# Optimization experiments

Hardware: AMD Instinct MI355X
Metric: run time of the kernel (lower is better)

## Reference

```python
import jax, jax.numpy as jnp
import numpy as np

T, N, F_IN, H, E, OUT = 24, 20000, 64, 256, 320000, 1


def setup_inputs() -> dict:
    key = jax.random.key(0)
    ks = jax.random.split(key, 16)
    inp = {
        "x": jax.random.normal(ks[0], (T, N, F_IN), dtype=jnp.float32),
        "edge_index": jax.random.randint(ks[1], (2, E), 0, N, dtype=jnp.int32),
        "edge_weight": jax.random.uniform(ks[2], (E,), dtype=jnp.float32),
        # GCNConv 1 (input_size -> hidden)
        "W1": jax.random.normal(ks[3], (F_IN, H), dtype=jnp.float32) / np.sqrt(F_IN),
        "b1": jnp.zeros((H,), dtype=jnp.float32),
        # GCNConv 2 (hidden -> hidden)
        "W2": jax.random.normal(ks[4], (H, H), dtype=jnp.float32) / np.sqrt(H),
        "b2": jnp.zeros((H,), dtype=jnp.float32),
        # LayerNorm affine
        "ln_w": jnp.ones((H,), dtype=jnp.float32),
        "ln_b": jnp.zeros((H,), dtype=jnp.float32),
        # GRU (1 layer): weight_ih [3H,H_in], weight_hh [3H,H]
        "Wih": jax.random.normal(ks[5], (3 * H, H), dtype=jnp.float32) / np.sqrt(H),
        "Whh": jax.random.normal(ks[6], (3 * H, H), dtype=jnp.float32) / np.sqrt(H),
        "bih": jnp.zeros((3 * H,), dtype=jnp.float32),
        "bhh": jnp.zeros((3 * H,), dtype=jnp.float32),
        # fc
        "Wfc": jax.random.normal(ks[7], (OUT, H), dtype=jnp.float32) / np.sqrt(H),
        "bfc": jnp.zeros((OUT,), dtype=jnp.float32),
    }
    return inp


def _gcn_norm(edge_index, edge_weight, n_nodes):
    # PyG gcn_norm with self-loops (fill=1.0) and symmetric normalization.
    loop = jnp.arange(n_nodes, dtype=edge_index.dtype)
    src = jnp.concatenate([edge_index[0], loop])
    dst = jnp.concatenate([edge_index[1], loop])
    ew = jnp.concatenate([edge_weight, jnp.ones((n_nodes,), edge_weight.dtype)])
    deg = jax.ops.segment_sum(ew, dst, num_segments=n_nodes)
    dinv = jnp.where(deg > 0, jax.lax.rsqrt(deg), 0.0)
    norm = dinv[src] * ew * dinv[dst]
    return src, dst, norm


def _gcn_conv(x, src, dst, norm, W, b, n_nodes):
    h = x @ W                              # [N, out]
    msg = norm[:, None] * h[src]           # [E+N, out]
    out = jax.ops.segment_sum(msg, dst, num_segments=n_nodes)
    return out + b


def reference(x, edge_index, edge_weight, W1, b1, W2, b2, ln_w, ln_b,
              Wih, Whh, bih, bhh, Wfc, bfc):
    n_nodes = x.shape[1]
    src, dst, norm = _gcn_norm(edge_index, edge_weight, n_nodes)

    def encode(xt):  # xt: [N, F_IN]
        h = _gcn_conv(xt, src, dst, norm, W1, b1, n_nodes)
        h = jnp.where(h >= 0, h, 0.01 * h)  # leaky_relu, slope 0.01
        h = _gcn_conv(h, src, dst, norm, W2, b2, n_nodes)
        mu = jnp.mean(h, axis=-1, keepdims=True)
        var = jnp.mean(jnp.square(h - mu), axis=-1, keepdims=True)
        return (h - mu) * jax.lax.rsqrt(var + 1e-5) * ln_w + ln_b

    seq = jax.vmap(encode)(x)  # [T, N, H]

    def gru_step(h, xt):
        gi = xt @ Wih.T + bih
        gh = h @ Whh.T + bhh
        ir, iz, inn = jnp.split(gi, 3, axis=-1)
        hr, hz, hn = jnp.split(gh, 3, axis=-1)
        r = jax.nn.sigmoid(ir + hr)
        z = jax.nn.sigmoid(iz + hz)
        n = jnp.tanh(inn + r * hn)
        h_new = (1.0 - z) * n + z * h
        return h_new, None

    h0 = jnp.zeros((n_nodes, Whh.shape[1]), dtype=x.dtype)
    h_last, _ = jax.lax.scan(gru_step, h0, seq)
    return h_last @ Wfc.T + bfc  # [N, OUT]
```

## Files before the change

### kernel.cpp

```cpp
#include <hip/hip_runtime.h>
#include <math.h>

#define T_STEPS 24
#define N_NODES 20000
#define F_IN 64
#define H_DIM 256
#define H3 (3 * H_DIM)
#define TC 4
#define NCHUNK (T_STEPS / TC)
#define GRU_BM_GRPS 160

using f16x8 = __attribute__((ext_vector_type(8))) _Float16;
using f16x4 = __attribute__((ext_vector_type(4))) _Float16;
using f16x2 = __attribute__((ext_vector_type(2))) _Float16;
using f32x4 = __attribute__((ext_vector_type(4))) float;

__device__ __forceinline__ void gload_lds16(const void* g, void* l) {
    __builtin_amdgcn_global_load_lds(
        (const __attribute__((address_space(1))) void*)(uintptr_t)g,
        (__attribute__((address_space(3))) void*)l, 16, 0, 0);
}

__device__ __forceinline__ float sigmoidf_(float x) { return 1.0f / (1.0f + expf(-x)); }

__global__ void init_deg_kernel(float* deg, int* indeg, int n) {
    int i = blockIdx.x * blockDim.x + threadIdx.x;
    if (i < n) { deg[i] = 1.0f; indeg[i] = 0; }
}

__global__ void accum_deg_kernel(const int* __restrict__ src, const int* __restrict__ dst,
                                 const float* __restrict__ ew, float* deg, int* indeg, int E) {
    int e = blockIdx.x * blockDim.x + threadIdx.x;
    if (e < E) {
        atomicAdd(&deg[dst[e]], ew[e]);
        atomicAdd(&indeg[dst[e]], 1);
    }
}

__global__ void dinv_kernel(float* deg, float* selfnorm, int n) {
    int i = blockIdx.x * blockDim.x + threadIdx.x;
    if (i < n) {
        float d = deg[i];
        float di = (d > 0.0f) ? rsqrtf(d) : 0.0f;
        deg[i] = di;
        selfnorm[i] = di * di;
    }
}

__global__ void edge_norm_kernel(const int* __restrict__ src, const int* __restrict__ dst,
                                 const float* __restrict__ ew, const float* __restrict__ dinv,
                                 float* norm, int E) {
    int e = blockIdx.x * blockDim.x + threadIdx.x;
    if (e < E) norm[e] = dinv[src[e]] * ew[e] * dinv[dst[e]];
}

__global__ void scan_kernel(const int* __restrict__ indeg, int* offs, int* cursor, int N) {
    __shared__ int part[1024];
    int t = threadIdx.x;
    const int CH = (N + 1023) / 1024;
    int s = 0;
    for (int i = 0; i < CH; i++) {
        int idx = t * CH + i;
        if (idx < N) s += indeg[idx];
    }
    part[t] = s;
    __syncthreads();
    for (int off = 1; off < 1024; off <<= 1) {
        int v = (t >= off) ? part[t - off] : 0;
        __syncthreads();
        part[t] += v;
        __syncthreads();
    }
    int base = (t == 0) ? 0 : part[t - 1];
    for (int i = 0; i < CH; i++) {
        int idx = t * CH + i;
        if (idx < N) {
            offs[idx] = base;
            cursor[idx] = base;
            base += indeg[idx];
        }
    }
    if (t == 0) offs[N] = part[1023];
}

__global__ void csr_fill_kernel(const int* __restrict__ src, const int* __restrict__ dst,
                                const float* __restrict__ norm, int* cursor,
                                int* csr_src, float* csr_norm, int E) {
    int e = blockIdx.x * blockDim.x + threadIdx.x;
    if (e < E) {
        int d = dst[e];
        int pos = atomicAdd(&cursor[d], 1);
        csr_src[pos] = src[e];
        csr_norm[pos] = norm[e];
    }
}

__global__ void pack_b16_kernel(const float* __restrict__ W, _Float16* __restrict__ P,
                                int K, int Nn, int trans) {
    int idx = blockIdx.x * blockDim.x + threadIdx.x;
    int total = (K >> 3) * Nn;
    if (idx >= total) return;
    int kk = idx / Nn, c = idx - kk * Nn;
    int n = c;
    if (trans == 2) {
        int a = c / 48, w = c % 48;
        int g = w >> 4, b = w & 15;
        n = g * 256 + a * 16 + b;
    }
    size_t o = (size_t)idx * 8;
    for (int j = 0; j < 8; ++j) {
        float v = (trans != 0) ? W[(size_t)n * K + kk * 8 + j] : W[(size_t)(kk * 8 + j) * Nn + n];
        P[o + j] = (_Float16)v;
    }
}

__global__ void perm_bias_kernel(const float* __restrict__ b, float* __restrict__ pb) {
    int c = blockIdx.x * blockDim.x + threadIdx.x;
    if (c < H3) {
        int a = c / 48, w = c % 48;
        int g = w >> 4, bb = w & 15;
        pb[c] = b[g * 256 + a * 16 + bb];
    }
}

__global__ void tofp16_kernel(const float* __restrict__ in, _Float16* __restrict__ out, int n4) {
    int i = blockIdx.x * blockDim.x + threadIdx.x;
    if (i < n4) {
        float4 v = ((const float4*)in)[i];
        f16x4 o = { (_Float16)v.x, (_Float16)v.y, (_Float16)v.z, (_Float16)v.w };
        ((f16x4*)out)[i] = o;
    }
}

__global__ void agg1_kernel(const _Float16* __restrict__ xs, const int* __restrict__ offs,
                            const int* __restrict__ csr_src, const float* __restrict__ csr_norm,
                            const float* __restrict__ selfnorm,
                            _Float16* __restrict__ out, int N) {
    int t = blockIdx.y;
    int n = blockIdx.x * 4 + (threadIdx.x >> 6);
    int lane = threadIdx.x & 63;
    int fg = lane & 7, ep = lane >> 3;
    const _Float16* xsl = xs + (size_t)t * N * F_IN;
    float acc[8] = {};
    int e0 = offs[n], e1 = offs[n + 1];
    int e = e0 + ep;
    for (; e + 8 < e1; e += 16) {
        int sA = csr_src[e], sB = csr_src[e + 8];
        float wA = csr_norm[e], wB = csr_norm[e + 8];
        f16x8 vA = *(const f16x8*)&xsl[(size_t)sA * F_IN + fg * 8];
        f16x8 vB = *(const f16x8*)&xsl[(size_t)sB * F_IN + fg * 8];
#pragma unroll
        for (int c = 0; c < 8; ++c) acc[c] = fmaf(wA, (float)vA[c], acc[c]);
#pragma unroll
        for (int c = 0; c < 8; ++c) acc[c] = fmaf(wB, (float)vB[c], acc[c]);
    }
    if (e < e1) {
        int s = csr_src[e];
        float w = csr_norm[e];
        f16x8 v = *(const f16x8*)&xsl[(size_t)s * F_IN + fg * 8];
#pragma unroll
        for (int c = 0; c < 8; ++c) acc[c] = fmaf(w, (float)v[c], acc[c]);
    }
#pragma unroll
    for (int c = 0; c < 8; ++c) {
        acc[c] += __shfl_xor(acc[c], 8, 64);
        acc[c] += __shfl_xor(acc[c], 16, 64);
        acc[c] += __shfl_xor(acc[c], 32, 64);
    }
    f16x8 own = *(const f16x8*)&xsl[(size_t)n * F_IN + fg * 8];
    float sn = selfnorm[n];
#pragma unroll
    for (int c = 0; c < 8; ++c) acc[c] = fmaf(sn, (float)own[c], acc[c]);
    if (ep == 0) {
        f16x8 o;
#pragma unroll
        for (int c = 0; c < 8; ++c) o[c] = (_Float16)acc[c];
        *(f16x8*)&out[((size_t)t * N + n) * F_IN + fg * 8] = o;
    }
}

__global__ void agg2_kernel(const _Float16* __restrict__ hs, const int* __restrict__ offs,
                            const int* __restrict__ csr_src, const float* __restrict__ csr_norm,
                            const float* __restrict__ selfnorm,
                            _Float16* __restrict__ out, int N) {
    int t = blockIdx.y;
    int n = blockIdx.x * 4 + (threadIdx.x >> 6);
    int lane = threadIdx.x & 63;
    int half = lane >> 5, fl = lane & 31;
    const _Float16* hsl = hs + (size_t)t * N * H_DIM;
    float acc[8] = {};
    int e0 = offs[n], e1 = offs[n + 1];
    int e = e0;
    for (; e + 8 <= e1; e += 8) {
        int eb = e + half * 4;
        int s0 = csr_src[eb], s1 = csr_src[eb + 1], s2 = csr_src[eb + 2], s3 = csr_src[eb + 3];
        float w0 = csr_norm[eb], w1 = csr_norm[eb + 1], w2 = csr_norm[eb + 2], w3 = csr_norm[eb + 3];
        f16x8 v0 = *(const f16x8*)&hsl[(size_t)s0 * H_DIM + fl * 8];
        f16x8 v1 = *(const f16x8*)&hsl[(size_t)s1 * H_DIM + fl * 8];
        f16x8 v2 = *(const f16x8*)&hsl[(size_t)s2 * H_DIM + fl * 8];
        f16x8 v3 = *(const f16x8*)&hsl[(size_t)s3 * H_DIM + fl * 8];
#pragma unroll
        for (int c = 0; c < 8; ++c) acc[c] = fmaf(w0, (float)v0[c], acc[c]);
#pragma unroll
        for (int c = 0; c < 8; ++c) acc[c] = fmaf(w1, (float)v1[c], acc[c]);
#pragma unroll
        for (int c = 0; c < 8; ++c) acc[c] = fmaf(w2, (float)v2[c], acc[c]);
#pragma unroll
        for (int c = 0; c < 8; ++c) acc[c] = fmaf(w3, (float)v3[c], acc[c]);
    }
    for (; e + 2 <= e1; e += 2) {
        int eb = e + half;
        int s = csr_src[eb];
        float w = csr_norm[eb];
        f16x8 v = *(const f16x8*)&hsl[(size_t)s * H_DIM + fl * 8];
#pragma unroll
        for (int c = 0; c < 8; ++c) acc[c] = fmaf(w, (float)v[c], acc[c]);
    }
    if (e < e1 && half == 0) {
        int s = csr_src[e];
        float w = csr_norm[e];
        f16x8 v = *(const f16x8*)&hsl[(size_t)s * H_DIM + fl * 8];
#pragma unroll
        for (int c = 0; c < 8; ++c) acc[c] = fmaf(w, (float)v[c], acc[c]);
    }
#pragma unroll
    for (int c = 0; c < 8; ++c) acc[c] += __shfl_xor(acc[c], 32, 64);
    f16x8 own = *(const f16x8*)&hsl[(size_t)n * H_DIM + fl * 8];
    float sn = selfnorm[n];
#pragma unroll
    for (int c = 0; c < 8; ++c) acc[c] = fmaf(sn, (float)own[c], acc[c]);
    if (half == 0) {
        f16x8 o;
#pragma unroll
        for (int c = 0; c < 8; ++c) o[c] = (_Float16)acc[c];
        *(f16x8*)&out[((size_t)t * N + n) * H_DIM + fl * 8] = o;
    }
}

__global__ __launch_bounds__(256, 4)
void conv1_kernel(const _Float16* __restrict__ A, const _Float16* __restrict__ Bp,
                  const float* __restrict__ bias, _Float16* __restrict__ C16,
                  int M, int Nn, int K) {
    __shared__ _Float16 As[4][128][8];
    __shared__ _Float16 Bs[4][128][8];

    const int tid = threadIdx.x;
    const int wave = tid >> 6, lane = tid & 63;
    const int bm = blockIdx.x * 128, bn = blockIdx.y * 128;
    const int wm = (wave >> 1) * 64, wn = (wave & 1) * 64;
    const int kq = lane >> 4, r = lane & 15;

    f32x4 acc[4][4];
#pragma unroll
    for (int i = 0; i < 4; ++i)
#pragma unroll
        for (int j = 0; j < 4; ++j) acc[i][j] = (f32x4){0.f, 0.f, 0.f, 0.f};

    for (int k0 = 0; k0 < K; k0 += 32) {
        __syncthreads();
        const int kb = k0 >> 3;
#pragma unroll
        for (int it = 0; it < 2; ++it) {
            int c = it * 256 + tid;
            int kk = c >> 7, idx = c & 127;
            int row = bm + idx;
            if (row >= M) row = M - 1;
            size_t aoff = (size_t)row * K + k0 + kk * 8;
            size_t boff = ((size_t)(kb + kk) * Nn + bn + idx) * 8;
            gload_lds16(A + aoff, &As[0][0][0] + (size_t)c * 8);
            gload_lds16(Bp + boff, &Bs[0][0][0] + (size_t)c * 8);
        }
        __syncthreads();

        f16x8 a[4], b[4];
#pragma unroll
        for (int f = 0; f < 4; ++f) {
            a[f] = *(const f16x8*)&As[kq][wm + f * 16 + r][0];
            b[f] = *(const f16x8*)&Bs[kq][wn + f * 16 + r][0];
        }
#pragma unroll
        for (int i = 0; i < 4; ++i)
#pragma unroll
            for (int j = 0; j < 4; ++j)
                acc[i][j] = __builtin_amdgcn_mfma_f32_16x16x32_f16(b[j], a[i], acc[i][j], 0, 0, 0);
    }

#pragma unroll
    for (int j = 0; j < 4; ++j) {
        int colb = bn + wn + j * 16 + kq * 4;
        float4 bv = *(const float4*)&bias[colb];
#pragma unroll
        for (int i = 0; i < 4; ++i) {
            int row = bm + wm + i * 16 + r;
            f16x4 o;
#pragma unroll
            for (int q = 0; q < 4; ++q) {
                float v = acc[i][j][q] + ((const float*)&bv)[q];
                v = (v >= 0.0f) ? v : 0.01f * v;
                o[q] = (_Float16)v;
            }
            *(f16x4*)&C16[(size_t)row * Nn + colb] = o;
        }
    }
}

__global__ __launch_bounds__(256, 2)
void conv2ln_kernel(const _Float16* __restrict__ A, const _Float16* __restrict__ Bp,
                    const float* __restrict__ b2, const float* __restrict__ lnw,
                    const float* __restrict__ lnb, _Float16* __restrict__ out, int M) {
    __shared__ _Float16 As[4][128][8];
    __shared__ _Float16 Bs[4][256][8];
    __shared__ float lnP[128][2][2];

    const int tid = threadIdx.x;
    const int wave = tid >> 6, lane = tid & 63;
    const int bm = blockIdx.x * 128;
    const int wm = (wave >> 1) * 64, wn = (wave & 1) * 128;
    const int cw = wave & 1;
    const int kq = lane >> 4, r = lane & 15;

    f32x4 acc[4][8];
#pragma unroll
    for (int i = 0; i < 4; ++i)
#pragma unroll
        for (int j = 0; j < 8; ++j) acc[i][j] = (f32x4){0.f, 0.f, 0.f, 0.f};

    for (int k0 = 0; k0 < H_DIM; k0 += 32) {
        __syncthreads();
        const int kb = k0 >> 3;
#pragma unroll
        for (int it = 0; it < 2; ++it) {
            int c = it * 256 + tid;
            int kk = c >> 7, idx = c & 127;
            int row = bm + idx;
            if (row >= M) row = M - 1;
            gload_lds16(A + (size_t)row * H_DIM + k0 + kk * 8, &As[0][0][0] + (size_t)c * 8);
        }
#pragma unroll
        for (int it = 0; it < 4; ++it) {
            int c = it * 256 + tid;
            int kk = c >> 8, col = c & 255;
            gload_lds16(Bp + ((size_t)(kb + kk) * H_DIM + col) * 8, &Bs[0][0][0] + (size_t)c * 8);
        }
        __syncthreads();

        f16x8 a[4], b[8];
#pragma unroll
        for (int f = 0; f < 4; ++f) a[f] = *(const f16x8*)&As[kq][wm + f * 16 + r][0];
#pragma unroll
        for (int f = 0; f < 8; ++f) b[f] = *(const f16x8*)&Bs[kq][wn + f * 16 + r][0];
#pragma unroll
        for (int i = 0; i < 4; ++i)
#pragma unroll
            for (int j = 0; j < 8; ++j)
                acc[i][j] = __builtin_amdgcn_mfma_f32_16x16x32_f16(b[j], a[i], acc[i][j], 0, 0, 0);
    }

#pragma unroll
    for (int i = 0; i < 4; ++i) {
        float s = 0.f, s2 = 0.f;
#pragma unroll
        for (int j = 0; j < 8; ++j) {
            float4 bv = *(const float4*)&b2[wn + j * 16 + kq * 4];
#pragma unroll
            for (int q = 0; q < 4; ++q) {
                float v = acc[i][j][q] + ((const float*)&bv)[q];
                acc[i][j][q] = v;
                s += v;
                s2 += v * v;
            }
        }
        s += __shfl_xor(s, 16, 64);  s2 += __shfl_xor(s2, 16, 64);
        s += __shfl_xor(s, 32, 64);  s2 += __shfl_xor(s2, 32, 64);
        int lrow = wm + i * 16 + r;
        if (kq == 0) { lnP[lrow][cw][0] = s; lnP[lrow][cw][1] = s2; }
    }
    __syncthreads();

#pragma unroll
    for (int i = 0; i < 4; ++i) {
        int lrow = wm + i * 16 + r;
        int row = bm + lrow;
        float S = lnP[lrow][0][0] + lnP[lrow][1][0];
        float S2 = lnP[lrow][0][1] + lnP[lrow][1][1];
        float mu = S * (1.0f / H_DIM);
        float var = S2 * (1.0f / H_DIM) - mu * mu;
        float rstd = rsqrtf(var + 1e-5f);
#pragma unroll
        for (int j = 0; j < 8; ++j) {
            int colb = wn + j * 16 + kq * 4;
            float4 wv = *(const float4*)&lnw[colb];
            float4 bvv = *(const float4*)&lnb[colb];
            f16x4 o;
#pragma unroll
            for (int q = 0; q < 4; ++q)
                o[q] = (_Float16)((acc[i][j][q] - mu) * rstd * ((const float*)&wv)[q] + ((const float*)&bvv)[q]);
            *(f16x4*)&out[(size_t)row * H_DIM + colb] = o;
        }
    }
}

__global__ __launch_bounds__(256, 3)
void gru_step_kernel(const _Float16* __restrict__ hprev, const _Float16* __restrict__ e,
                     const _Float16* __restrict__ Bhh, const _Float16* __restrict__ Bih,
                     const float* __restrict__ pbhh, const float* __restrict__ pbih,
                     _Float16* __restrict__ hnew, int M) {
    const int bid = blockIdx.x;
    const int bn_grp = bid / GRU_BM_GRPS;
    const int bm_grp = bid - bn_grp * GRU_BM_GRPS;
    if (bm_grp * 128 >= M) return;
    const int bm = bm_grp * 128, bn = bn_grp * 96;

    __shared__ _Float16 Ah[4][128][8];
    __shared__ _Float16 Ae[4][128][8];
    __shared__ _Float16 Bsh[4][96][8];
    __shared__ _Float16 Bsi[4][96][8];

    const int tid = threadIdx.x;
    const int wave = tid >> 6, lane = tid & 63;
    const int wm = (wave >> 1) * 64, wn = (wave & 1) * 48;
    const int kq = lane >> 4, r = lane & 15;

    f32x4 arz[4][2], ahn[4], ainn[4];
#pragma unroll
    for (int i = 0; i < 4; ++i) {
        arz[i][0] = (f32x4){0.f, 0.f, 0.f, 0.f};
        arz[i][1] = (f32x4){0.f, 0.f, 0.f, 0.f};
        ahn[i] = (f32x4){0.f, 0.f, 0.f, 0.f};
        ainn[i] = (f32x4){0.f, 0.f, 0.f, 0.f};
    }

    for (int k0 = 0; k0 < H_DIM; k0 += 32) {
        __syncthreads();
        const int kb = k0 >> 3;
#pragma unroll
        for (int it = 0; it < 2; ++it) {
            int c = it * 256 + tid;
            int kk = c >> 7, idx = c & 127;
            int row = bm + idx;
            if (row >= M) row = M - 1;
            size_t ao = (size_t)row * H_DIM + k0 + kk * 8;
            gload_lds16(hprev + ao, &Ah[0][0][0] + (size_t)c * 8);
            gload_lds16(e + ao, &Ae[0][0][0] + (size_t)c * 8);
        }
        {
            int c = tid;
            int kk = c / 96, col = c - kk * 96;
            size_t bo = ((size_t)(kb + kk) * H3 + bn + col) * 8;
            gload_lds16(Bhh + bo, &Bsh[0][0][0] + (size_t)c * 8);
            gload_lds16(Bih + bo, &Bsi[0][0][0] + (size_t)c * 8);
            if (tid < 128) {
                int c2 = 256 + tid;
                int kk2 = c2 / 96, col2 = c2 - kk2 * 96;
                size_t bo2 = ((size_t)(kb + kk2) * H3 + bn + col2) * 8;
                gload_lds16(Bhh + bo2, &Bsh[0][0][0] + (size_t)c2 * 8);
                gload_lds16(Bih + bo2, &Bsi[0][0][0] + (size_t)c2 * 8);
            }
        }
        __syncthreads();

        f16x8 ah[4], ae[4], bh[3], bi[3];
#pragma unroll
        for (int f = 0; f < 4; ++f) {
            ah[f] = *(const f16x8*)&Ah[kq][wm + f * 16 + r][0];
            ae[f] = *(const f16x8*)&Ae[kq][wm + f * 16 + r][0];
        }
#pragma unroll
        for (int f = 0; f < 3; ++f) {
            bh[f] = *(const f16x8*)&Bsh[kq][wn + f * 16 + r][0];
            bi[f] = *(const f16x8*)&Bsi[kq][wn + f * 16 + r][0];
        }
#pragma unroll
        for (int i = 0; i < 4; ++i) {
            arz[i][0] = __builtin_amdgcn_mfma_f32_16x16x32_f16(bh[0], ah[i], arz[i][0], 0, 0, 0);
            arz[i][0] = __builtin_amdgcn_mfma_f32_16x16x32_f16(bi[0], ae[i], arz[i][0], 0, 0, 0);
            arz[i][1] = __builtin_amdgcn_mfma_f32_16x16x32_f16(bh[1], ah[i], arz[i][1], 0, 0, 0);
            arz[i][1] = __builtin_amdgcn_mfma_f32_16x16x32_f16(bi[1], ae[i], arz[i][1], 0, 0, 0);
            ahn[i] = __builtin_amdgcn_mfma_f32_16x16x32_f16(bh[2], ah[i], ahn[i], 0, 0, 0);
            ainn[i] = __builtin_amdgcn_mfma_f32_16x16x32_f16(bi[2], ae[i], ainn[i], 0, 0, 0);
        }
    }

    const int colbase = bn + wn;
    const int agrp = colbase / 48;
    const int fb = agrp * 16 + kq * 4;
    float b_r[4], b_z[4], b_hn[4], b_in[4];
#pragma unroll
    for (int q = 0; q < 4; ++q) {
        int cq = colbase + kq * 4 + q;
        b_r[q]  = pbhh[cq] + pbih[cq];
        b_z[q]  = pbhh[cq + 16] + pbih[cq + 16];
        b_hn[q] = pbhh[cq + 32];
        b_in[q] = pbih[cq + 32];
    }
#pragma unroll
    for (int i = 0; i < 4; ++i) {
        int row = bm + wm + i * 16 + r;
        if (row < M) {
            f16x4 hp = *(const f16x4*)&hprev[(size_t)row * H_DIM + fb];
            f16x4 o;
#pragma unroll
            for (int q = 0; q < 4; ++q) {
                float rg = sigmoidf_(arz[i][0][q] + b_r[q]);
                float zg = sigmoidf_(arz[i][1][q] + b_z[q]);
                float nn = tanhf(ainn[i][q] + b_in[q] + rg * (ahn[i][q] + b_hn[q]));
                o[q] = (_Float16)((1.0f - zg) * nn + zg * (float)hp[q]);
            }
            *(f16x4*)&hnew[(size_t)row * H_DIM + fb] = o;
        }
    }
}

__global__ void fc_kernel(const _Float16* __restrict__ h, const float* __restrict__ Wfc,
                          const float* __restrict__ bfc, float* __restrict__ out, int N) {
    int n = blockIdx.x * 4 + (threadIdx.x >> 6);
    int lane = threadIdx.x & 63;
    if (n >= N) return;
    f16x4 hv = *(const f16x4*)&h[(size_t)n * H_DIM + lane * 4];
    float4 wv = *(const float4*)&Wfc[lane * 4];
    float acc = (float)hv[0] * wv.x + (float)hv[1] * wv.y + (float)hv[2] * wv.z + (float)hv[3] * wv.w;
#pragma unroll
    for (int o = 32; o > 0; o >>= 1) acc += __shfl_down(acc, o, 64);
    if (lane == 0) out[n] = acc + bfc[0];
}

extern "C" void kernel_launch(void* const* d_in, const int* in_sizes, int n_in,
                              void* d_out, int out_size, void* d_ws, size_t ws_size,
                              hipStream_t stream) {
    const float* x   = (const float*)d_in[0];
    const int* eidx  = (const int*)d_in[1];
    const float* ew  = (const float*)d_in[2];
    const float* W1  = (const float*)d_in[3];
    const float* b1  = (const float*)d_in[4];
    const float* W2  = (const float*)d_in[5];
    const float* b2  = (const float*)d_in[6];
    const float* lnw = (const float*)d_in[7];
    const float* lnb = (const float*)d_in[8];
    const float* Wih = (const float*)d_in[9];
    const float* Whh = (const float*)d_in[10];
    const float* bih = (const float*)d_in[11];
    const float* bhh = (const float*)d_in[12];
    const float* Wfc = (const float*)d_in[13];
    const float* bfc = (const float*)d_in[14];

    const int E = in_sizes[2];
    const int N = N_NODES;
    const int* src = eidx;
    const int* dst = eidx + E;

    uintptr_t p = (uintptr_t)d_ws;
    auto alloc = [&](size_t bytes) -> void* {
        p = (p + 255) & ~(uintptr_t)255;
        void* r = (void*)p;
        p += bytes;
        return r;
    };
    float* deg      = (float*)alloc(N * sizeof(float));
    float* selfnorm = (float*)alloc(N * sizeof(float));
    float* norm     = (float*)alloc(E * sizeof(float));
    int* indeg      = (int*)alloc(N * sizeof(int));
    int* offs       = (int*)alloc((N + 1) * sizeof(int));
    int* cursor     = (int*)alloc(N * sizeof(int));
    int* csr_src    = (int*)alloc(E * sizeof(int));
    float* csr_norm = (float*)alloc(E * sizeof(float));
    _Float16* W1p   = (_Float16*)alloc((size_t)F_IN * H_DIM * sizeof(_Float16));
    _Float16* W2p   = (_Float16*)alloc((size_t)H_DIM * H_DIM * sizeof(_Float16));
    _Float16* Wihp  = (_Float16*)alloc((size_t)H_DIM * H3 * sizeof(_Float16));
    _Float16* Whhp  = (_Float16*)alloc((size_t)H_DIM * H3 * sizeof(_Float16));
    float* pbih     = (float*)alloc(H3 * sizeof(float));
    float* pbhh     = (float*)alloc(H3 * sizeof(float));
    _Float16* xs16  = (_Float16*)alloc((size_t)TC * N * F_IN * sizeof(_Float16));
    _Float16* a1_16 = (_Float16*)alloc((size_t)TC * N * F_IN * sizeof(_Float16));
    _Float16* h1_16 = (_Float16*)alloc((size_t)TC * N * H_DIM * sizeof(_Float16));
    _Float16* a2_16 = (_Float16*)alloc((size_t)TC * N * H_DIM * sizeof(_Float16));
    _Float16* e16   = (_Float16*)alloc((size_t)TC * N * H_DIM * sizeof(_Float16));
    _Float16* h_a   = (_Float16*)alloc((size_t)N * H_DIM * sizeof(_Float16));
    _Float16* h_b   = (_Float16*)alloc((size_t)N * H_DIM * sizeof(_Float16));

    const int TB = 256;
    hipLaunchKernelGGL(init_deg_kernel, dim3((N + TB - 1) / TB), dim3(TB), 0, stream, deg, indeg, N);
    hipLaunchKernelGGL(accum_deg_kernel, dim3((E + TB - 1) / TB), dim3(TB), 0, stream, src, dst, ew, deg, indeg, E);
    hipLaunchKernelGGL(dinv_kernel, dim3((N + TB - 1) / TB), dim3(TB), 0, stream, deg, selfnorm, N);
    hipLaunchKernelGGL(edge_norm_kernel, dim3((E + TB - 1) / TB), dim3(TB), 0, stream, src, dst, ew, deg, norm, E);
    hipLaunchKernelGGL(scan_kernel, dim3(1), dim3(1024), 0, stream, indeg, offs, cursor, N);
    hipLaunchKernelGGL(csr_fill_kernel, dim3((E + TB - 1) / TB), dim3(TB), 0, stream, src, dst, norm, cursor, csr_src, csr_norm, E);

    {
        int tot = (F_IN / 8) * H_DIM;
        hipLaunchKernelGGL(pack_b16_kernel, dim3((tot + TB - 1) / TB), dim3(TB), 0, stream, W1, W1p, F_IN, H_DIM, 0);
        tot = (H_DIM / 8) * H_DIM;
        hipLaunchKernelGGL(pack_b16_kernel, dim3((tot + TB - 1) / TB), dim3(TB), 0, stream, W2, W2p, H_DIM, H_DIM, 0);
        tot = (H_DIM / 8) * H3;
        hipLaunchKernelGGL(pack_b16_kernel, dim3((tot + TB - 1) / TB), dim3(TB), 0, stream, Wih, Wihp, H_DIM, H3, 2);
        hipLaunchKernelGGL(pack_b16_kernel, dim3((tot + TB - 1) / TB), dim3(TB), 0, stream, Whh, Whhp, H_DIM, H3, 2);
        hipLaunchKernelGGL(perm_bias_kernel, dim3((H3 + TB - 1) / TB), dim3(TB), 0, stream, bih, pbih);
        hipLaunchKernelGGL(perm_bias_kernel, dim3((H3 + TB - 1) / TB), dim3(TB), 0, stream, bhh, pbhh);
    }

    hipMemsetAsync(h_a, 0, (size_t)N * H_DIM * sizeof(_Float16), stream);

    const int MC = TC * N;
    dim3 gb(256);
    dim3 g_conv1(MC / 128, H_DIM / 128);
    dim3 g_c2ln(MC / 128);
    dim3 g_gru(8 * GRU_BM_GRPS);
    dim3 g_agg(N / 4, TC);

    _Float16* h_cur = h_a;
    _Float16* h_nxt = h_b;

    for (int chunk = 0; chunk < NCHUNK; ++chunk) {
        const float* xc = x + (size_t)chunk * TC * N * F_IN;
        int n4 = TC * N * F_IN / 4;
        hipLaunchKernelGGL(tofp16_kernel, dim3((n4 + TB - 1) / TB), dim3(TB), 0, stream, xc, xs16, n4);
        hipLaunchKernelGGL(agg1_kernel, g_agg, dim3(256), 0, stream,
                           xs16, offs, csr_src, csr_norm, selfnorm, a1_16, N);
        hipLaunchKernelGGL(conv1_kernel, g_conv1, gb, 0, stream,
                           a1_16, W1p, b1, h1_16, MC, H_DIM, F_IN);
        hipLaunchKernelGGL(agg2_kernel, g_agg, dim3(256), 0, stream,
                           h1_16, offs, csr_src, csr_norm, selfnorm, a2_16, N);
        hipLaunchKernelGGL(conv2ln_kernel, g_c2ln, gb, 0, stream,
                           a2_16, W2p, b2, lnw, lnb, e16, MC);
        for (int tc = 0; tc < TC; ++tc) {
            hipLaunchKernelGGL(gru_step_kernel, g_gru, gb, 0, stream,
                               h_cur, e16 + (size_t)tc * N * H_DIM, Whhp, Wihp,
                               pbhh, pbih, h_nxt, N);
            _Float16* tmp = h_cur; h_cur = h_nxt; h_nxt = tmp;
        }
    }

    hipLaunchKernelGGL(fc_kernel, dim3((N + 3) / 4), dim3(256), 0, stream, h_cur, Wfc, bfc, (float*)d_out, N);
}
```

Before: 2.176 ms.

## Split agg2 gather into column slices with eight edges per wave

The second-layer aggregation is restructured so that each block handles one 32-column slice of a group of 4 nodes (8 slices per node) across a flattened 1D grid. Within a wave, 8 lanes cover 4 columns each while 8 edge groups process edges in parallel, followed by a 3-step shuffle reduction. The intent is more parallelism and more outstanding gathers per node with smaller per-lane loads. In exchange it issues 8x more blocks, rereads the CSR indices and weights once per slice, and uses narrower 8-byte loads.

```diff
diff --git a/kernel.cpp b/kernel.cpp
--- a/kernel.cpp
+++ b/kernel.cpp
@@ -183,57 +183,49 @@
                             const int* __restrict__ csr_src, const float* __restrict__ csr_norm,
                             const float* __restrict__ selfnorm,
                             _Float16* __restrict__ out, int N) {
-    int t = blockIdx.y;
-    int n = blockIdx.x * 4 + (threadIdx.x >> 6);
+    int id = blockIdx.x;
+    int cs = id & 7;
+    int rest = id >> 3;
+    int ngrp = rest % (N_NODES / 4);
+    int t = rest / (N_NODES / 4);
+    int n = ngrp * 4 + (threadIdx.x >> 6);
     int lane = threadIdx.x & 63;
-    int half = lane >> 5, fl = lane & 31;
+    int fg = lane & 7, ep = lane >> 3;
+    int col = cs * 32 + fg * 4;
     const _Float16* hsl = hs + (size_t)t * N * H_DIM;
-    float acc[8] = {};
+    f32x4 acc = (f32x4){0.f, 0.f, 0.f, 0.f};
     int e0 = offs[n], e1 = offs[n + 1];
-    int e = e0;
-    for (; e + 8 <= e1; e += 8) {
-        int eb = e + half * 4;
-        int s0 = csr_src[eb], s1 = csr_src[eb + 1], s2 = csr_src[eb + 2], s3 = csr_src[eb + 3];
-        float w0 = csr_norm[eb], w1 = csr_norm[eb + 1], w2 = csr_norm[eb + 2], w3 = csr_norm[eb + 3];
-        f16x8 v0 = *(const f16x8*)&hsl[(size_t)s0 * H_DIM + fl * 8];
-        f16x8 v1 = *(const f16x8*)&hsl[(size_t)s1 * H_DIM + fl * 8];
-        f16x8 v2 = *(const f16x8*)&hsl[(size_t)s2 * H_DIM + fl * 8];
-        f16x8 v3 = *(const f16x8*)&hsl[(size_t)s3 * H_DIM + fl * 8];
-#pragma unroll
-        for (int c = 0; c < 8; ++c) acc[c] = fmaf(w0, (float)v0[c], acc[c]);
-#pragma unroll
-        for (int c = 0; c < 8; ++c) acc[c] = fmaf(w1, (float)v1[c], acc[c]);
-#pragma unroll
-        for (int c = 0; c < 8; ++c) acc[c] = fmaf(w2, (float)v2[c], acc[c]);
-#pragma unroll
-        for (int c = 0; c < 8; ++c) acc[c] = fmaf(w3, (float)v3[c], acc[c]);
-    }
-    for (; e + 2 <= e1; e += 2) {
-        int eb = e + half;
-        int s = csr_src[eb];
-        float w = csr_norm[eb];
-        f16x8 v = *(const f16x8*)&hsl[(size_t)s * H_DIM + fl * 8];
-#pragma unroll
-        for (int c = 0; c < 8; ++c) acc[c] = fmaf(w, (float)v[c], acc[c]);
-    }
-    if (e < e1 && half == 0) {
+    int e = e0 + ep;
+    for (; e + 8 < e1; e += 16) {
+        int sA = csr_src[e], sB = csr_src[e + 8];
+        float wA = csr_norm[e], wB = csr_norm[e + 8];
+        f16x4 vA = *(const f16x4*)&hsl[(size_t)sA * H_DIM + col];
+        f16x4 vB = *(const f16x4*)&hsl[(size_t)sB * H_DIM + col];
+#pragma unroll
+        for (int c = 0; c < 4; ++c) acc[c] = fmaf(wA, (float)vA[c], acc[c]);
+#pragma unroll
+        for (int c = 0; c < 4; ++c) acc[c] = fmaf(wB, (float)vB[c], acc[c]);
+    }
+    if (e < e1) {
         int s = csr_src[e];
         float w = csr_norm[e];
-        f16x8 v = *(const f16x8*)&hsl[(size_t)s * H_DIM + fl * 8];
-#pragma unroll
-        for (int c = 0; c < 8; ++c) acc[c] = fmaf(w, (float)v[c], acc[c]);
-    }
-#pragma unroll
-    for (int c = 0; c < 8; ++c) acc[c] += __shfl_xor(acc[c], 32, 64);
-    f16x8 own = *(const f16x8*)&hsl[(size_t)n * H_DIM + fl * 8];
+        f16x4 v = *(const f16x4*)&hsl[(size_t)s * H_DIM + col];
+#pragma unroll
+        for (int c = 0; c < 4; ++c) acc[c] = fmaf(w, (float)v[c], acc[c]);
+    }
+#pragma unroll
+    for (int c = 0; c < 4; ++c) {
+        acc[c] += __shfl_xor(acc[c], 8, 64);
+        acc[c] += __shfl_xor(acc[c], 16, 64);
+        acc[c] += __shfl_xor(acc[c], 32, 64);
+    }
+    f16x4 own = *(const f16x4*)&hsl[(size_t)n * H_DIM + col];
     float sn = selfnorm[n];
 #pragma unroll
-    for (int c = 0; c < 8; ++c) acc[c] = fmaf(sn, (float)own[c], acc[c]);
-    if (half == 0) {
-        f16x8 o;
-#pragma unroll
-        for (int c = 0; c < 8; ++c) o[c] = (_Float16)acc[c];
-        *(f16x8*)&out[((size_t)t * N + n) * H_DIM + fl * 8] = o;
+    for (int c = 0; c < 4; ++c) acc[c] = fmaf(sn, (float)own[c], acc[c]);
+    if (ep == 0) {
+        f16x4 o = { (_Float16)acc[0], (_Float16)acc[1], (_Float16)acc[2], (_Float16)acc[3] };
+        *(f16x4*)&out[((size_t)t * N + n) * H_DIM + col] = o;
     }
 }
 
@@ -604,7 +596,8 @@
     dim3 g_conv1(MC / 128, H_DIM / 128);
     dim3 g_c2ln(MC / 128);
     dim3 g_gru(8 * GRU_BM_GRPS);
-    dim3 g_agg(N / 4, TC);
+    dim3 g_agg1(N / 4, TC);
+    dim3 g_agg2((N / 4) * 8 * TC);
 
     _Float16* h_cur = h_a;
     _Float16* h_nxt = h_b;
@@ -613,11 +606,11 @@
         const float* xc = x + (size_t)chunk * TC * N * F_IN;
         int n4 = TC * N * F_IN / 4;
         hipLaunchKernelGGL(tofp16_kernel, dim3((n4 + TB - 1) / TB), dim3(TB), 0, stream, xc, xs16, n4);
-        hipLaunchKernelGGL(agg1_kernel, g_agg, dim3(256), 0, stream,
+        hipLaunchKernelGGL(agg1_kernel, g_agg1, dim3(256), 0, stream,
                            xs16, offs, csr_src, csr_norm, selfnorm, a1_16, N);
         hipLaunchKernelGGL(conv1_kernel, g_conv1, gb, 0, stream,
                            a1_16, W1p, b1, h1_16, MC, H_DIM, F_IN);
-        hipLaunchKernelGGL(agg2_kernel, g_agg, dim3(256), 0, stream,
+        hipLaunchKernelGGL(agg2_kernel, g_agg2, dim3(256), 0, stream,
                            h1_16, offs, csr_src, csr_norm, selfnorm, a2_16, N);
         hipLaunchKernelGGL(conv2ln_kernel, g_c2ln, gb, 0, stream,
                            a2_16, W2p, b2, lnw, lnb, e16, MC);
```

New measurement: 2.911 ms. +33.8%, slower.
